# Kernel optimization log

Measured on AMD Instinct MI355X. Metric: run time of the kernel, lower is better.

## Reference

```python
import jax, jax.numpy as jnp
import numpy as np

B, T, C, H = 8, 2048, 768, 12
D = C // H

def setup_inputs() -> dict:
    key = jax.random.key(0)
    ks = jax.random.split(key, 5)
    s = 0.02
    return {
        "x": jax.random.normal(ks[0], (B, T, C), dtype=jnp.float32),
        "w_attn": jax.random.normal(ks[1], (C, 3 * C), dtype=jnp.float32) * s,
        "b_attn": jnp.zeros((3 * C,), dtype=jnp.float32),
        "w_proj": jax.random.normal(ks[2], (C, C), dtype=jnp.float32) * s,
        "b_proj": jnp.zeros((C,), dtype=jnp.float32),
    }

def reference(x, w_attn, b_attn, w_proj, b_proj):
    Bx, Tx, Cx = x.shape
    qkv = x @ w_attn + b_attn                       # [B,T,3C]
    q, k, v = jnp.split(qkv, 3, axis=-1)
    # [B,H,T,D]
    q = q.reshape(Bx, Tx, H, D).transpose(0, 2, 1, 3)
    k = k.reshape(Bx, Tx, H, D).transpose(0, 2, 1, 3)
    v = v.reshape(Bx, Tx, H, D).transpose(0, 2, 1, 3)
    scale = 1.0 / jnp.sqrt(jnp.float32(D))
    att = jnp.einsum('bhqd,bhkd->bhqk', q, k) * scale
    causal = jnp.tril(jnp.ones((Tx, Tx), dtype=bool))
    att = jnp.where(causal[None, None], att, -jnp.inf)
    att = jax.nn.softmax(att, axis=-1)
    y = jnp.einsum('bhqk,bhkd->bhqd', att, v)
    y = y.transpose(0, 2, 1, 3).reshape(Bx, Tx, Cx)
    y = y @ w_proj + b_proj
    return y, k, v
```

## Files before the change

kernel.cpp:

```cpp
#include <hip/hip_runtime.h>
#include <hip/hip_bf16.h>
#include <stdint.h>

#define Bz 8
#define Tz 2048
#define Cz 768
#define Hz 12
#define Dz 64
#define Mz (Bz*Tz)
#define N3 (3*Cz)
#define YSZ ((size_t)Mz*Cz)

#define SCL 0.18033688011112042f
#define KVB 64
#define QBLK 256

typedef __bf16 bf16;
typedef __attribute__((ext_vector_type(8))) bf16 bf16x8;
typedef __attribute__((ext_vector_type(4))) bf16 bf16x4;
typedef __attribute__((ext_vector_type(4))) float f32x4;

#define MFMA(A_,B_,C_) __builtin_amdgcn_mfma_f32_16x16x32_bf16(A_,B_,C_,0,0,0)

__device__ __forceinline__ void gll16(const void* g, void* l) {
  __builtin_amdgcn_global_load_lds(
      (const __attribute__((address_space(1))) void*)g,
      (__attribute__((address_space(3))) void*)l, 16, 0, 0);
}

__global__ __launch_bounds__(256) void prep_x(const float* __restrict__ x,
                                              bf16* __restrict__ xb) {
  int i = blockIdx.x*blockDim.x + threadIdx.x;
  int stride = gridDim.x*blockDim.x;
  const float4* x4 = (const float4*)x;
  int n8 = (int)(YSZ/8);
  for (int j = i; j < n8; j += stride) {
    float4 f0 = x4[2*j];
    float4 f1 = x4[2*j + 1];
    bf16x8 o = { (bf16)f0.x, (bf16)f0.y, (bf16)f0.z, (bf16)f0.w,
                 (bf16)f1.x, (bf16)f1.y, (bf16)f1.z, (bf16)f1.w };
    *(bf16x8*)(xb + 8*(size_t)j) = o;
  }
}

__global__ __launch_bounds__(256) void transpose_conv(const float* __restrict__ src,
                                                      bf16* __restrict__ dst,
                                                      int R, int Ncol) {
  __shared__ float tile[32][33];
  int bx = blockIdx.x, by = blockIdx.y;
  int tx = threadIdx.x & 31, ty = threadIdx.x >> 5;
  #pragma unroll
  for (int i = 0; i < 4; ++i)
    tile[ty + 8*i][tx] = src[(size_t)(by*32 + ty + 8*i)*Ncol + bx*32 + tx];
  __syncthreads();
  #pragma unroll
  for (int i = 0; i < 4; ++i)
    dst[(size_t)(bx*32 + ty + 8*i)*R + by*32 + tx] = (bf16)tile[tx][ty + 8*i];
}

template<int EPI>
__global__ __launch_bounds__(256) void gemm128(
    const bf16* __restrict__ A, const bf16* __restrict__ Bt,
    int Kdim, int Mtiles, int Ntiles,
    const float* __restrict__ bias,
    bf16* __restrict__ qws, bf16* __restrict__ kws, bf16* __restrict__ vtb,
    float* __restrict__ kout, float* __restrict__ vout,
    float* __restrict__ yout)
{
  __shared__ alignas(16) bf16 sA[2][128*64];
  __shared__ alignas(16) bf16 sB[2][128*64];
  int nwg = Mtiles*Ntiles;
  int bid = blockIdx.x;
  int cpx = nwg >> 3;
  int swz = (bid & 7)*cpx + (bid >> 3);
  int ntile = swz % Ntiles, mtile = swz / Ntiles;
  int tid = threadIdx.x, w = tid >> 6, l = tid & 63;
  int wr = w >> 1, wc = w & 1;
  const int rowBase = mtile*128, colBase = ntile*128;

  f32x4 acc[4][4] = {};

  int rbase = tid >> 3;
  int ch    = tid & 7;
  int swk   = (ch ^ (rbase & 7)) << 3;
  const bf16* gA = A + (size_t)(rowBase + rbase)*Kdim + swk;
  const bf16* gB = Bt + (size_t)(colBase + rbase)*Kdim + swk;

  int lr = l & 15, lg = l >> 4;
  int nK = Kdim >> 6;

  {
    char* lA = (char*)sA[0] + w*1024;
    char* lB = (char*)sB[0] + w*1024;
    #pragma unroll
    for (int p = 0; p < 4; ++p) {
      gll16(gA + (size_t)(p*32)*Kdim, lA + p*4096);
      gll16(gB + (size_t)(p*32)*Kdim, lB + p*4096);
    }
    gA += 64; gB += 64;
  }
  int buf = 0;
  for (int t = 0; t < nK; ++t) {
    if (t + 1 < nK) {
      char* lA = (char*)sA[buf ^ 1] + w*1024;
      char* lB = (char*)sB[buf ^ 1] + w*1024;
      #pragma unroll
      for (int p = 0; p < 4; ++p) {
        gll16(gA + (size_t)(p*32)*Kdim, lA + p*4096);
        gll16(gB + (size_t)(p*32)*Kdim, lB + p*4096);
      }
      gA += 64; gB += 64;
      asm volatile("s_waitcnt vmcnt(8)" ::: "memory");
    } else {
      asm volatile("s_waitcnt vmcnt(0)" ::: "memory");
    }
    __builtin_amdgcn_s_barrier();
    __builtin_amdgcn_sched_barrier(0);
    const char* cA = (const char*)sA[buf];
    const char* cB = (const char*)sB[buf];
    __builtin_amdgcn_s_setprio(1);
    #pragma unroll
    for (int kk = 0; kk < 2; ++kk) {
      bf16x8 af[4], bfr[4];
      int cc = ((kk*4 + lg) ^ (lr & 7)) << 4;
      #pragma unroll
      for (int m = 0; m < 4; ++m)
        af[m] = *(const bf16x8*)(cA + (wr*64 + m*16 + lr)*128 + cc);
      #pragma unroll
      for (int n = 0; n < 4; ++n)
        bfr[n] = *(const bf16x8*)(cB + (wc*64 + n*16 + lr)*128 + cc);
      #pragma unroll
      for (int m = 0; m < 4; ++m)
        #pragma unroll
        for (int n = 0; n < 4; ++n)
          acc[m][n] = MFMA(af[m], bfr[n], acc[m][n]);
    }
    __builtin_amdgcn_s_setprio(0);
    asm volatile("s_waitcnt lgkmcnt(0)" ::: "memory");
    __builtin_amdgcn_s_barrier();
    __builtin_amdgcn_sched_barrier(0);
    buf ^= 1;
  }

  #pragma unroll
  for (int m = 0; m < 4; ++m) {
    #pragma unroll
    for (int n = 0; n < 4; ++n) {
      int gcol = colBase + wc*64 + n*16 + lr;
      float bv = bias[gcol];
      int grow0 = rowBase + wr*64 + m*16 + lg*4;
      if (EPI == 1) {
        #pragma unroll
        for (int r = 0; r < 4; ++r)
          yout[(size_t)(grow0 + r)*Cz + gcol] = acc[m][n][r] + bv;
      } else {
        int which = gcol / Cz;
        int within = gcol - which*Cz;
        int h = within >> 6, d = within & 63;
        int bidx = grow0 >> 11;
        int t0 = grow0 & 2047;
        size_t bhTD = ((size_t)bidx*Hz + h);
        if (which == 0) {
          bf16* qp = qws + (bhTD*Tz + t0)*Dz + d;
          #pragma unroll
          for (int r = 0; r < 4; ++r)
            qp[(size_t)r*Dz] = (bf16)((acc[m][n][r] + bv) * SCL);
        } else if (which == 1) {
          float* kp = kout + (bhTD*Tz + t0)*Dz + d;
          bf16*  kp2 = kws + (bhTD*Tz + t0)*Dz + d;
          #pragma unroll
          for (int r = 0; r < 4; ++r) {
            float v = acc[m][n][r] + bv;
            kp[(size_t)r*Dz] = v;
            kp2[(size_t)r*Dz] = (bf16)v;
          }
        } else {
          float* vp = vout + (bhTD*Tz + t0)*Dz + d;
          bf16x4 pk;
          #pragma unroll
          for (int r = 0; r < 4; ++r) {
            float v = acc[m][n][r] + bv;
            vp[(size_t)r*Dz] = v;
            pk[r] = (bf16)v;
          }
          int ts = (t0 & ~31) | (((t0 >> 2) & 3) << 3) | (((t0 >> 4) & 1) << 2) | (t0 & 3);
          *(bf16x4*)(vtb + (bhTD*Dz + d)*Tz + ts) = pk;
        }
      }
    }
  }
}

__device__ __forceinline__ void attn_tile(
    int kv0, int qminw, int qmaxw, int q_l, int lr, int lg,
    const char* cK, const char* cV,
    const bf16x8& qf0, const bf16x8& qf1, const bf16x8& ones,
    f32x4 (&o)[4], f32x4& lsum)
{
  const f32x4 zf = {0.f, 0.f, 0.f, 0.f};
  f32x4 s[4];
  __builtin_amdgcn_s_setprio(1);
  #pragma unroll
  for (int n = 0; n < 4; ++n) {
    int kvb = kv0 + n*16;
    if (kvb <= qmaxw) {
      int row = n*16 + lr;
      int c0 = lg ^ (lr & 7);
      bf16x8 kf0 = *(const bf16x8*)(cK + row*128 + (c0 << 4));
      bf16x8 kf1 = *(const bf16x8*)(cK + row*128 + ((c0 ^ 4) << 4));
      f32x4 t = MFMA(kf0, qf0, zf);
      s[n] = MFMA(kf1, qf1, t);
    } else {
      s[n][0] = -1e30f; s[n][1] = -1e30f; s[n][2] = -1e30f; s[n][3] = -1e30f;
    }
  }
  __builtin_amdgcn_s_setprio(0);
  #pragma unroll
  for (int n = 0; n < 4; ++n) {
    int kvb = kv0 + n*16;
    if (kvb <= qmaxw && kvb + 15 > qminw) {
      #pragma unroll
      for (int r = 0; r < 4; ++r)
        s[n][r] = (kvb + 4*lg + r <= q_l) ? s[n][r] : -1e30f;
    }
  }
  #pragma unroll
  for (int n = 0; n < 4; ++n) {
    #pragma unroll
    for (int r = 0; r < 4; ++r)
      s[n][r] = exp2f(s[n][r]);
  }
  __builtin_amdgcn_s_setprio(1);
  #pragma unroll
  for (int kk = 0; kk < 2; ++kk) {
    if (kv0 + kk*32 <= qmaxw) {
      bf16x8 pf;
      pf[0] = (bf16)s[2*kk][0];   pf[1] = (bf16)s[2*kk][1];
      pf[2] = (bf16)s[2*kk][2];   pf[3] = (bf16)s[2*kk][3];
      pf[4] = (bf16)s[2*kk+1][0]; pf[5] = (bf16)s[2*kk+1][1];
      pf[6] = (bf16)s[2*kk+1][2]; pf[7] = (bf16)s[2*kk+1][3];
      lsum = MFMA(pf, ones, lsum);
      int cb = (kk*4 + lg) ^ (lr & 7);
      #pragma unroll
      for (int nd = 0; nd < 4; ++nd) {
        bf16x8 vf = *(const bf16x8*)(cV + (nd*16 + lr)*128 + (cb << 4));
        o[nd] = MFMA(pf, vf, o[nd]);
      }
    }
  }
  __builtin_amdgcn_s_setprio(0);
}

__global__ __launch_bounds__(1024, 4) void attn128(
    const bf16* __restrict__ qws, const bf16* __restrict__ kb,
    const bf16* __restrict__ vtb, bf16* __restrict__ yatt)
{
  __shared__ alignas(16) char sK[2][8192];
  __shared__ alignas(16) char sV[2][8192];
  int bid = blockIdx.x;
  int qb = (Tz/QBLK) - 1 - bid/(Bz*Hz);
  int bh = bid % (Bz*Hz);
  int b = bh / Hz, h = bh - b*Hz;
  int tid = threadIdx.x, w = tid >> 6, l = tid & 63;
  int lr = l & 15, lg = l >> 4;
  const int q0 = qb*QBLK;
  const int qminw = q0 + w*16;
  const int qmaxw = qminw + 15;
  const int q_l = qminw + lr;

  const bf16* qbase = qws + ((size_t)bh*Tz + qminw + lr)*Dz + lg*8;
  bf16x8 qf0 = *(const bf16x8*)qbase;
  bf16x8 qf1 = *(const bf16x8*)(qbase + 32);

  bf16 onev = (bf16)1.0f;
  bf16x8 ones = { onev, onev, onev, onev, onev, onev, onev, onev };

  f32x4 o[4] = {};
  f32x4 lsum = {0.f, 0.f, 0.f, 0.f};

  bool isK = tid < 512;
  int soff = (tid & 511) * 16;
  int srow = soff >> 7;
  int sch  = (soff >> 4) & 7;
  int ssw  = ((sch ^ (srow & 7)) << 3);
  const bf16* sp = isK ? (kb  + (size_t)bh*Tz*Dz + (size_t)srow*Dz + ssw)
                       : (vtb + (size_t)bh*Dz*Tz + (size_t)srow*Tz + ssw);
  ptrdiff_t sstride = isK ? (ptrdiff_t)KVB*Dz : (ptrdiff_t)KVB;
  char* d0 = isK ? (sK[0] + w*1024) : (sV[0] + (w - 8)*1024);
  char* d1 = isK ? (sK[1] + w*1024) : (sV[1] + (w - 8)*1024);

  int nT = 4*qb + 4;
  gll16(sp, d0); sp += sstride;

  int buf = 0;
  for (int kt = 0; kt < nT; ++kt) {
    if (kt + 1 < nT) {
      gll16(sp, buf ? d0 : d1); sp += sstride;
      asm volatile("s_waitcnt vmcnt(1)" ::: "memory");
    } else {
      asm volatile("s_waitcnt vmcnt(0)" ::: "memory");
    }
    __builtin_amdgcn_s_barrier();
    __builtin_amdgcn_sched_barrier(0);
    attn_tile(kt*KVB, qminw, qmaxw, q_l, lr, lg, sK[buf], sV[buf],
              qf0, qf1, ones, o, lsum);
    if (kt + 1 < nT) {
      asm volatile("s_waitcnt lgkmcnt(0)" ::: "memory");
      __builtin_amdgcn_s_barrier();
      __builtin_amdgcn_sched_barrier(0);
    }
    buf ^= 1;
  }

  f32x4 inv;
  #pragma unroll
  for (int r = 0; r < 4; ++r) inv[r] = 1.0f / lsum[r];
  #pragma unroll
  for (int nd = 0; nd < 4; ++nd) {
    int d = nd*16 + lr;
    int t0 = q0 + w*16 + lg*4;
    bf16* yp = yatt + ((size_t)(b*Tz + t0))*Cz + h*Dz + d;
    yp[0*Cz]   = (bf16)(o[nd][0] * inv[0]);
    yp[1*Cz]   = (bf16)(o[nd][1] * inv[1]);
    yp[2*Cz]   = (bf16)(o[nd][2] * inv[2]);
    yp[3*Cz]   = (bf16)(o[nd][3] * inv[3]);
  }
}

extern "C" void kernel_launch(void* const* d_in, const int* in_sizes, int n_in,
                              void* d_out, int out_size, void* d_ws, size_t ws_size,
                              hipStream_t stream) {
  const float* x      = (const float*)d_in[0];
  const float* w_attn = (const float*)d_in[1];
  const float* b_attn = (const float*)d_in[2];
  const float* w_proj = (const float*)d_in[3];
  const float* b_proj = (const float*)d_in[4];

  float* y    = (float*)d_out;
  float* kout = y + YSZ;
  float* vout = y + 2*YSZ;

  char* ws = (char*)d_ws;
  bf16* xb   = (bf16*)ws;
  bf16* qws  = (bf16*)(ws + 25165824);
  bf16* kb   = (bf16*)(ws + 50331648);
  bf16* vtb  = (bf16*)(ws + 75497472);
  bf16* wtA  = (bf16*)(ws + 100663296);
  bf16* wtP  = (bf16*)(ws + 104202240);
  bf16* yatt = xb;

  prep_x<<<2048, 256, 0, stream>>>(x, xb);
  transpose_conv<<<dim3(N3/32, Cz/32), 256, 0, stream>>>(w_attn, wtA, Cz, N3);
  transpose_conv<<<dim3(Cz/32, Cz/32), 256, 0, stream>>>(w_proj, wtP, Cz, Cz);

  gemm128<0><<<dim3((Mz/128)*(N3/128)), 256, 0, stream>>>(
      xb, wtA, Cz, Mz/128, N3/128, b_attn, qws, kb, vtb, kout, vout, nullptr);

  attn128<<<dim3((Tz/QBLK)*(Bz*Hz)), 1024, 0, stream>>>(qws, kb, vtb, yatt);

  gemm128<1><<<dim3((Mz/128)*(Cz/128)), 256, 0, stream>>>(
      yatt, wtP, Cz, Mz/128, Cz/128, b_proj, nullptr, nullptr, nullptr,
      nullptr, nullptr, y);
}
```

Baseline: 258.3 us.

## Enlarge GEMM tiles to 256x128 with triple-buffered LDS staging

Both GEMMs move from 128x128 tiles with 256 threads to 256x128 tiles with 512 threads (8 waves), so each B tile is reused across more rows. Global-to-LDS prefetch becomes three-stage, two K-tiles ahead, with matching vmcnt waits. This is meant to cut global traffic per FLOP and hide load latency better. The cost is about 144KB of LDS per block, which limits each CU to one block, and coarser grids, especially the 384-block projection GEMM, which may balance poorly across CUs. Separately, the attention tile function now returns early when a KV tile lies entirely above the causal diagonal.

```diff
diff --git a/kernel.cpp b/kernel.cpp
--- a/kernel.cpp
+++ b/kernel.cpp
@@ -59,7 +59,7 @@
 }
 
 template<int EPI>
-__global__ __launch_bounds__(256) void gemm128(
+__global__ __launch_bounds__(512) void gemm256x128(
     const bf16* __restrict__ A, const bf16* __restrict__ Bt,
     int Kdim, int Mtiles, int Ntiles,
     const float* __restrict__ bias,
@@ -67,8 +67,8 @@
     float* __restrict__ kout, float* __restrict__ vout,
     float* __restrict__ yout)
 {
-  __shared__ alignas(16) bf16 sA[2][128*64];
-  __shared__ alignas(16) bf16 sB[2][128*64];
+  __shared__ alignas(16) bf16 sA[3][256*64];
+  __shared__ alignas(16) bf16 sB[3][128*64];
   int nwg = Mtiles*Ntiles;
   int bid = blockIdx.x;
   int cpx = nwg >> 3;
@@ -76,7 +76,7 @@
   int ntile = swz % Ntiles, mtile = swz / Ntiles;
   int tid = threadIdx.x, w = tid >> 6, l = tid & 63;
   int wr = w >> 1, wc = w & 1;
-  const int rowBase = mtile*128, colBase = ntile*128;
+  const int rowBase = mtile*256, colBase = ntile*128;
 
   f32x4 acc[4][4] = {};
 
@@ -89,35 +89,36 @@
   int lr = l & 15, lg = l >> 4;
   int nK = Kdim >> 6;
 
-  {
-    char* lA = (char*)sA[0] + w*1024;
-    char* lB = (char*)sB[0] + w*1024;
-    #pragma unroll
-    for (int p = 0; p < 4; ++p) {
-      gll16(gA + (size_t)(p*32)*Kdim, lA + p*4096);
-      gll16(gB + (size_t)(p*32)*Kdim, lB + p*4096);
-    }
-    gA += 64; gB += 64;
-  }
-  int buf = 0;
+  auto stage = [&](int t, int s) {
+    const bf16* a = gA + (size_t)t*64;
+    const bf16* b = gB + (size_t)t*64;
+    char* lA = (char*)sA[s] + tid*16;
+    char* lB = (char*)sB[s] + tid*16;
+    gll16(a,                      lA);
+    gll16(a + (size_t)64*Kdim,    lA + 8192);
+    gll16(a + (size_t)128*Kdim,   lA + 16384);
+    gll16(a + (size_t)192*Kdim,   lA + 24576);
+    gll16(b,                      lB);
+    gll16(b + (size_t)64*Kdim,    lB + 8192);
+  };
+
+  stage(0, 0);
+  if (nK > 1) stage(1, 1);
+
   for (int t = 0; t < nK; ++t) {
-    if (t + 1 < nK) {
-      char* lA = (char*)sA[buf ^ 1] + w*1024;
-      char* lB = (char*)sB[buf ^ 1] + w*1024;
-      #pragma unroll
-      for (int p = 0; p < 4; ++p) {
-        gll16(gA + (size_t)(p*32)*Kdim, lA + p*4096);
-        gll16(gB + (size_t)(p*32)*Kdim, lB + p*4096);
-      }
-      gA += 64; gB += 64;
-      asm volatile("s_waitcnt vmcnt(8)" ::: "memory");
+    int cur = t % 3;
+    if (t + 2 < nK) {
+      stage(t + 2, (t + 2) % 3);
+      asm volatile("s_waitcnt vmcnt(12)" ::: "memory");
+    } else if (t + 1 < nK) {
+      asm volatile("s_waitcnt vmcnt(6)" ::: "memory");
     } else {
       asm volatile("s_waitcnt vmcnt(0)" ::: "memory");
     }
     __builtin_amdgcn_s_barrier();
     __builtin_amdgcn_sched_barrier(0);
-    const char* cA = (const char*)sA[buf];
-    const char* cB = (const char*)sB[buf];
+    const char* cA = (const char*)sA[cur];
+    const char* cB = (const char*)sB[cur];
     __builtin_amdgcn_s_setprio(1);
     #pragma unroll
     for (int kk = 0; kk < 2; ++kk) {
@@ -139,7 +140,6 @@
     asm volatile("s_waitcnt lgkmcnt(0)" ::: "memory");
     __builtin_amdgcn_s_barrier();
     __builtin_amdgcn_sched_barrier(0);
-    buf ^= 1;
   }
 
   #pragma unroll
@@ -197,6 +197,7 @@
     const bf16x8& qf0, const bf16x8& qf1, const bf16x8& ones,
     f32x4 (&o)[4], f32x4& lsum)
 {
+  if (kv0 > qmaxw) return;
   const f32x4 zf = {0.f, 0.f, 0.f, 0.f};
   f32x4 s[4];
   __builtin_amdgcn_s_setprio(1);
@@ -353,12 +354,12 @@
   transpose_conv<<<dim3(N3/32, Cz/32), 256, 0, stream>>>(w_attn, wtA, Cz, N3);
   transpose_conv<<<dim3(Cz/32, Cz/32), 256, 0, stream>>>(w_proj, wtP, Cz, Cz);
 
-  gemm128<0><<<dim3((Mz/128)*(N3/128)), 256, 0, stream>>>(
-      xb, wtA, Cz, Mz/128, N3/128, b_attn, qws, kb, vtb, kout, vout, nullptr);
+  gemm256x128<0><<<dim3((Mz/256)*(N3/128)), 512, 0, stream>>>(
+      xb, wtA, Cz, Mz/256, N3/128, b_attn, qws, kb, vtb, kout, vout, nullptr);
 
   attn128<<<dim3((Tz/QBLK)*(Bz*Hz)), 1024, 0, stream>>>(qws, kb, vtb, yatt);
 
-  gemm128<1><<<dim3((Mz/128)*(Cz/128)), 256, 0, stream>>>(
-      yatt, wtP, Cz, Mz/128, Cz/128, b_proj, nullptr, nullptr, nullptr,
+  gemm256x128<1><<<dim3((Mz/256)*(Cz/128)), 512, 0, stream>>>(
+      yatt, wtP, Cz, Mz/256, Cz/128, b_proj, nullptr, nullptr, nullptr,
       nullptr, nullptr, y);
 }
```

New measurement: 277.1 us. 1.07x slower.
